# Kernel tuning notes

Measured on AMD Instinct MI355X. Metric: run time of the kernel, lower is better.

Reference implementation:

```python
import jax, jax.numpy as jnp
import numpy as np
from jax import lax


def conv2d(x, w, b, stride=1, pad=0):
    y = lax.conv_general_dilated(x, w, (stride, stride), [(pad, pad), (pad, pad)],
                                 dimension_numbers=('NCHW', 'OIHW', 'NCHW'))
    return y + b[None, :, None, None]


def squash(s, axis):
    # v = (|s|^2 / (1+|s|^2)) * s / |s|
    sq = jnp.sum(s * s, axis=axis, keepdims=True)
    return (sq / (1.0 + sq)) * s / jnp.sqrt(sq + 1e-9)


def conv_capsule(x, w, b_conv, caps_bias, out_dim, out_atoms, num_routing, stride, pad):
    # x: [B, in_dim, in_atoms, H, W]
    B, in_dim, in_atoms, H, W = x.shape
    xr = x.reshape(B * in_dim, in_atoms, H, W)
    conv = conv2d(xr, w, b_conv, stride, pad)              # [B*in_dim, out_dim*out_atoms, Ho, Wo]
    Ho, Wo = conv.shape[-2], conv.shape[-1]
    votes = conv.reshape(B, in_dim, out_dim, out_atoms, Ho, Wo)
    logits = jnp.zeros((B, in_dim, out_dim, Ho, Wo), dtype=x.dtype)
    act = None
    for i in range(num_routing):  # num_routing is a small static int (1 or 3)
        route = jax.nn.softmax(logits, axis=2)             # coupling over output capsules
        preact = jnp.einsum('bioHW,bioaHW->boaHW', route, votes) + caps_bias[None]
        act = squash(preact, axis=2)                        # [B, out_dim, out_atoms, Ho, Wo]
        if i < num_routing - 1:
            logits = logits + jnp.einsum('bioaHW,boaHW->bioHW', votes, act)
    return act


def forward(x, y, W1, b1, Wp, bp, cbp, Ws, bs, cbs, Wr1, br1, Wr2, br2, Wr3, br3):
    conv1 = jax.nn.relu(conv2d(x, W1, b1, 1, 2))                       # [B,256,H,W]
    primary = conv_capsule(conv1[:, None], Wp, bp, cbp, 32, 8, 1, 1, 2)  # [B,32,8,H,W]
    seg = conv_capsule(primary, Ws, bs, cbs, 1, 16, 3, 1, 0)             # [B,1,16,H,W]
    out_seg = jnp.sqrt(jnp.sum(seg * seg, axis=2) + 1e-9)                # Length: [B,1,H,W]
    masked = seg * y[:, :, None]                                         # Mask by label
    B, C, A, H, W = masked.shape
    r = masked.reshape(B * C, A, H, W)                                   # [B,16,H,W]
    r = jax.nn.relu(conv2d(r, Wr1, br1))
    r = jax.nn.relu(conv2d(r, Wr2, br2))
    out_recon = jax.nn.sigmoid(conv2d(r, Wr3, br3))                      # [B,1,H,W]
    return out_seg, out_recon


def setup_inputs():
    key = jax.random.key(0)
    ks = jax.random.split(key, 10)
    B, H, W = 2, 128, 128
    s = 0.05
    return {
        'x': jax.random.uniform(ks[0], (B, 1, H, W), jnp.float32),
        'y': (jax.random.uniform(ks[1], (B, 1, H, W)) > 0.5).astype(jnp.float32),
        'W1': jax.random.normal(ks[2], (256, 1, 5, 5), jnp.float32) * s,
        'b1': jnp.zeros((256,), jnp.float32),
        'Wp': jax.random.normal(ks[3], (256, 256, 5, 5), jnp.float32) * 0.01,
        'bp': jnp.zeros((256,), jnp.float32),
        'cbp': jnp.full((32, 8, 1, 1), 0.1, jnp.float32),
        'Ws': jax.random.normal(ks[4], (16, 8, 1, 1), jnp.float32) * s,
        'bs': jnp.zeros((16,), jnp.float32),
        'cbs': jnp.full((1, 16, 1, 1), 0.1, jnp.float32),
        'Wr1': jax.random.normal(ks[5], (64, 16, 1, 1), jnp.float32) * s,
        'br1': jnp.zeros((64,), jnp.float32),
        'Wr2': jax.random.normal(ks[6], (128, 64, 1, 1), jnp.float32) * s,
        'br2': jnp.zeros((128,), jnp.float32),
        'Wr3': jax.random.normal(ks[7], (1, 128, 1, 1), jnp.float32) * s,
        'br3': jnp.zeros((1,), jnp.float32),
    }


def reference(x, y, W1, b1, Wp, bp, cbp, Ws, bs, cbs, Wr1, br1, Wr2, br2, Wr3, br3):
    return forward(x, y, W1, b1, Wp, bp, cbp, Ws, bs, cbs, Wr1, br1, Wr2, br2, Wr3, br3)
```

## Files before the change

### kernel.cpp

```cpp
#include <hip/hip_runtime.h>
#include <hip/hip_bf16.h>

typedef __attribute__((ext_vector_type(8))) unsigned short us8;
typedef __attribute__((ext_vector_type(8))) __bf16 bf16x8;
typedef __attribute__((ext_vector_type(4))) float f32x4;

__device__ __forceinline__ unsigned short f2bf(float f) {
  unsigned int u = __float_as_uint(f);
  u += 0x7FFFu + ((u >> 16) & 1u);
  return (unsigned short)(u >> 16);
}
__device__ __forceinline__ float bf2f(unsigned short u) {
  return __uint_as_float(((unsigned int)u) << 16);
}

__device__ __forceinline__ void gld16(const unsigned short* g, unsigned short* l) {
  __builtin_amdgcn_global_load_lds(reinterpret_cast<const unsigned int*>(g),
                                   reinterpret_cast<unsigned int*>(l), 16, 0, 0);
}

#define APAD_BYTES 17842176
#define BT_OFF     17842176
#define PP_OFF     21118976

__global__ __launch_bounds__(256) void halo_zero(unsigned short* __restrict__ Apad) {
  int idx = blockIdx.x * 256 + threadIdx.x;
  int t8 = idx & 31;
  int pix = idx >> 5;
  int hw = pix % 17424;
  int h = hw / 132, w = hw - h * 132;
  if (h < 2 || h >= 130 || w < 2 || w >= 130) {
    us8 z = {0, 0, 0, 0, 0, 0, 0, 0};
    *(us8*)(Apad + (size_t)pix * 256 + t8 * 8) = z;
  }
}

__global__ __launch_bounds__(256) void prep_w(const float* __restrict__ Wp,
                                              unsigned short* __restrict__ BT) {
  __shared__ float w[6400];
  const int n = blockIdx.x;
  const float* src = Wp + n * 6400;
  for (int i = threadIdx.x; i < 6400; i += 256) w[i] = src[i];
  __syncthreads();
  for (int k = threadIdx.x; k < 6400; k += 256) {
    int dhw = k >> 8, c = k & 255;
    BT[n * 6400 + k] = f2bf(w[c * 25 + dhw]);
  }
}

__global__ __launch_bounds__(256) void conv1_k(const float* __restrict__ x,
                                               const float* __restrict__ W1,
                                               const float* __restrict__ b1,
                                               unsigned short* __restrict__ Apad) {
  int t = threadIdx.x;
  int pxt = blockIdx.x >> 3;
  int cq  = blockIdx.x & 7;
  int px  = (pxt << 6) + (t & 63);
  int cg  = __builtin_amdgcn_readfirstlane(t >> 6);
  int co0 = (cq << 5) + (cg << 3);
  int b = px >> 14, hw = px & 16383;
  int h = hw >> 7, w = hw & 127;

  float patch[25];
#pragma unroll
  for (int dh = 0; dh < 5; ++dh)
#pragma unroll
    for (int dw = 0; dw < 5; ++dw) {
      int hh = h + dh - 2, ww = w + dw - 2;
      bool ok = (hh >= 0) & (hh < 128) & (ww >= 0) & (ww < 128);
      patch[dh * 5 + dw] = ok ? x[(b << 14) + hh * 128 + ww] : 0.f;
    }
  us8 o;
#pragma unroll
  for (int c = 0; c < 8; ++c) {
    float acc = b1[co0 + c];
#pragma unroll
    for (int i = 0; i < 25; ++i) acc += patch[i] * W1[(co0 + c) * 25 + i];
    o[c] = f2bf(fmaxf(acc, 0.f));
  }
  *(us8*)(Apad + (size_t)((b * 132 + h + 2) * 132 + (w + 2)) * 256 + co0) = o;
}

#define STAGE_A(slot, ku) do { int dhw_=(ku)>>3, dh_=dhw_/5, dw_=dhw_-dh_*5;   \
    int ao_=((dh_*132+dw_)<<8)+(((ku)&7)<<5);                                  \
    gld16(Aap+abase0+ao_, &As[slot][sA]);                                      \
    gld16(Aap+abase1+ao_, &As[slot][sA+4096]); } while(0)
#define STAGE_B(slot, ku) do { int kp_=(ku)<<5;                                \
    gld16(BT+bbase0+kp_, &Bs[slot][sA]);                                       \
    gld16(BT+bbase1+kp_, &Bs[slot][sA+4096]); } while(0)
#define RDA(slot, s) (*(const bf16x8*)(&As[slot][areadbase + (s)*512]))
#define RDB(slot, j) (*(const bf16x8*)(&Bs[slot][breadbase + (j)*512]))
#define MFMA_Q(aset, bset, rb) do {                                            \
  _Pragma("unroll") for (int s_ = 0; s_ < 4; ++s_)                             \
  _Pragma("unroll") for (int j_ = 0; j_ < 4; ++j_)                             \
    acc[(rb)+s_][j_] = __builtin_amdgcn_mfma_f32_16x16x32_bf16(                \
        aset[s_], bset[j_], acc[(rb)+s_][j_], 0, 0, 0); } while(0)
#define BAR() __builtin_amdgcn_s_barrier()
#define VMC(n) asm volatile("s_waitcnt vmcnt(" #n ")" ::: "memory")

__global__ __launch_bounds__(512, 2) void caps_conv2(
    const unsigned short* __restrict__ Aap,
    const unsigned short* __restrict__ BT,
    unsigned short* __restrict__ Pp)
{
  __shared__ __attribute__((aligned(16))) unsigned short As[4][8192];
  __shared__ __attribute__((aligned(16))) unsigned short Bs[4][8192];

  const int tid = threadIdx.x;
  const int bid = blockIdx.x;
  const int lid = (bid & 7) * 32 + (bid >> 3);
  const int kid = lid & 1;
  const int m0 = (lid >> 1) << 8;
  const int t0 = kid * 100;
  const int wid = tid >> 6;
  const int l = tid & 63;

  const int swz = (l & 3) ^ ((l >> 3) & 3);
  int abase0, abase1, bbase0, bbase1;
  {
    int ra = wid * 16 + (l >> 2);
    int m = m0 + ra;
    int b = m >> 14, hw = m & 16383, h = hw >> 7, w = hw & 127;
    abase0 = ((b * 132 + h) * 132 + w) * 256 + swz * 8;
    m = m0 + ra + 128;
    b = m >> 14; hw = m & 16383; h = hw >> 7; w = hw & 127;
    abase1 = ((b * 132 + h) * 132 + w) * 256 + swz * 8;
    bbase0 = ra * 6400 + swz * 8;
    bbase1 = (ra + 128) * 6400 + swz * 8;
  }
  const int sA = wid * 512;

  const int rl = l & 15, q = l >> 4;
  const int wm = wid >> 2, wn = wid & 3;
  const int areadbase = (wm * 128 + rl) * 32 + ((q ^ ((rl >> 1) & 3)) << 3);
  const int breadbase = (wn * 64 + rl) * 32 + ((q ^ ((rl >> 1) & 3)) << 3);

  f32x4 acc[8][4] = {};
  bf16x8 aL[2][4], aH[4], bB[2][4];

  STAGE_A(0, t0 + 0); STAGE_B(0, t0 + 0);
  STAGE_A(1, t0 + 1); STAGE_B(1, t0 + 1);
  STAGE_A(2, t0 + 2); STAGE_B(2, t0 + 2);
  VMC(8); BAR();
#pragma unroll
  for (int s = 0; s < 4; ++s) aL[0][s] = RDA(0, s);
#pragma unroll
  for (int j = 0; j < 4; ++j) bB[0][j] = RDB(0, j);

  for (int it = 0; it < 24; ++it) {
    const int ub = t0 + it * 4;
#pragma unroll
    for (int sub = 0; sub < 4; ++sub) {
      const int par = sub & 1, nxt = par ^ 1;
      const int sU = sub, sU1 = (sub + 1) & 3, sS = (sub + 3) & 3;
#pragma unroll
      for (int s = 0; s < 4; ++s) aH[s] = RDA(sU, 4 + s);
      STAGE_A(sS, ub + sub + 3);
      VMC(6); BAR();
      __builtin_amdgcn_s_setprio(1);
      MFMA_Q(aL[par], bB[par], 0);
      __builtin_amdgcn_s_setprio(0);
      BAR();
#pragma unroll
      for (int s = 0; s < 4; ++s) aL[nxt][s] = RDA(sU1, s);
#pragma unroll
      for (int j = 0; j < 4; ++j) bB[nxt][j] = RDB(sU1, j);
      STAGE_B(sS, ub + sub + 3);
      BAR();
      __builtin_amdgcn_s_setprio(1);
      MFMA_Q(aH, bB[par], 4);
      __builtin_amdgcn_s_setprio(0);
      BAR();
    }
  }

#pragma unroll
  for (int s = 0; s < 4; ++s) aH[s] = RDA(0, 4 + s);
  STAGE_A(3, t0 + 99);
  VMC(6); BAR();
  __builtin_amdgcn_s_setprio(1); MFMA_Q(aL[0], bB[0], 0);
  __builtin_amdgcn_s_setprio(0); BAR();
#pragma unroll
  for (int s = 0; s < 4; ++s) aL[1][s] = RDA(1, s);
#pragma unroll
  for (int j = 0; j < 4; ++j) bB[1][j] = RDB(1, j);
  STAGE_B(3, t0 + 99);
  BAR();
  __builtin_amdgcn_s_setprio(1); MFMA_Q(aH, bB[0], 4);
  __builtin_amdgcn_s_setprio(0); BAR();
#pragma unroll
  for (int s = 0; s < 4; ++s) aH[s] = RDA(1, 4 + s);
  VMC(4); BAR();
  MFMA_Q(aL[1], bB[1], 0); BAR();
#pragma unroll
  for (int s = 0; s < 4; ++s) aL[0][s] = RDA(2, s);
#pragma unroll
  for (int j = 0; j < 4; ++j) bB[0][j] = RDB(2, j);
  BAR();
  MFMA_Q(aH, bB[1], 4); BAR();
#pragma unroll
  for (int s = 0; s < 4; ++s) aH[s] = RDA(2, 4 + s);
  VMC(0); BAR();
  MFMA_Q(aL[0], bB[0], 0); BAR();
#pragma unroll
  for (int s = 0; s < 4; ++s) aL[1][s] = RDA(3, s);
#pragma unroll
  for (int j = 0; j < 4; ++j) bB[1][j] = RDB(3, j);
  BAR();
  MFMA_Q(aH, bB[0], 4); BAR();
#pragma unroll
  for (int s = 0; s < 4; ++s) aH[s] = RDA(3, 4 + s);
  MFMA_Q(aL[1], bB[1], 0);
  MFMA_Q(aH, bB[1], 4);

  unsigned short* P = Pp + kid * 8388608;
#pragma unroll
  for (int s = 0; s < 8; ++s) {
#pragma unroll
    for (int j = 0; j < 4; ++j) {
      int col = wn * 64 + j * 16 + rl;
      int mrow = m0 + wm * 128 + s * 16 + (q << 2);
#pragma unroll
      for (int e = 0; e < 4; ++e)
        P[(size_t)(mrow + e) * 256 + col] = f2bf(acc[s][j][e]);
    }
  }
}

__global__ __launch_bounds__(128) void tail_k2(
    const unsigned short* __restrict__ Pp, const float* __restrict__ y,
    const float* __restrict__ bp, const float* __restrict__ cbp,
    const float* __restrict__ Ws, const float* __restrict__ bs,
    const float* __restrict__ cbs,
    const float* __restrict__ Wr1, const float* __restrict__ br1,
    const float* __restrict__ Wr2, const float* __restrict__ br2,
    const float* __restrict__ Wr3, const float* __restrict__ br3,
    float* __restrict__ out) {
  __shared__ float ccl[256];
  __shared__ float sbl[16];
  __shared__ float Wsl[128];
  __shared__ float W1l[1024];
  __shared__ float b1l[64];
  __shared__ float W2l[8192];
  __shared__ float b2l[128];
  __shared__ float W3l[128];

  const int tid = threadIdx.x;
  for (int i = tid; i < 256; i += 128) ccl[i] = bp[i] * (1.f / 32.f) + cbp[i];
  if (tid < 16) sbl[tid] = 32.f * bs[tid] + cbs[tid];
  if (tid < 128) { Wsl[tid] = Ws[tid]; b2l[tid] = br2[tid]; W3l[tid] = Wr3[tid]; }
  if (tid < 64) b1l[tid] = br1[tid];
  for (int i = tid; i < 1024; i += 128) W1l[i] = Wr1[i];
  for (int i = tid; i < 8192; i += 128) W2l[i] = Wr2[i];
  __syncthreads();

  const int m = blockIdx.x * 128 + tid;
  const us8* pr0 = (const us8*)(Pp + (size_t)m * 256);
  const us8* pr1 = (const us8*)(Pp + 8388608 + (size_t)m * 256);

  float P8[8] = {0.f, 0.f, 0.f, 0.f, 0.f, 0.f, 0.f, 0.f};
#pragma unroll 4
  for (int i = 0; i < 32; ++i) {
    us8 a = pr0[i], b = pr1[i];
    float v[8];
    float sq = 0.f;
#pragma unroll
    for (int c = 0; c < 8; ++c) {
      v[c] = (bf2f(a[c]) + bf2f(b[c])) * (1.f / 32.f) + ccl[i * 8 + c];
      sq += v[c] * v[c];
    }
    float scale = sq / ((1.f + sq) * sqrtf(sq + 1e-9f));
#pragma unroll
    for (int c = 0; c < 8; ++c) P8[c] += v[c] * scale;
  }

  float pre[16];
  float sq2 = 0.f;
#pragma unroll
  for (int a = 0; a < 16; ++a) {
    float s = sbl[a];
#pragma unroll
    for (int c = 0; c < 8; ++c) s += P8[c] * Wsl[a * 8 + c];
    pre[a] = s;
    sq2 += s * s;
  }
  float sc2 = sq2 / ((1.f + sq2) * sqrtf(sq2 + 1e-9f));
  out[m] = sqrtf(sq2 * sc2 * sc2 + 1e-9f);

  const float f = sc2 * y[m];
  float r1v[64];
#pragma unroll
  for (int j = 0; j < 64; ++j) {
    float s = b1l[j];
#pragma unroll
    for (int a = 0; a < 16; ++a) s += pre[a] * f * W1l[j * 16 + a];
    r1v[j] = fmaxf(s, 0.f);
  }
  float acc2 = br3[0];
  for (int k = 0; k < 128; ++k) {
    float s = b2l[k];
    const float4* wrow = (const float4*)(W2l + k * 64);
#pragma unroll
    for (int jj = 0; jj < 16; ++jj) {
      float4 wv = wrow[jj];
      s += r1v[jj * 4 + 0] * wv.x + r1v[jj * 4 + 1] * wv.y +
           r1v[jj * 4 + 2] * wv.z + r1v[jj * 4 + 3] * wv.w;
    }
    acc2 += fmaxf(s, 0.f) * W3l[k];
  }
  out[32768 + m] = 1.f / (1.f + expf(-acc2));
}

extern "C" void kernel_launch(void* const* d_in, const int* in_sizes, int n_in,
                              void* d_out, int out_size, void* d_ws, size_t ws_size,
                              hipStream_t stream) {
  const float* x   = (const float*)d_in[0];
  const float* y   = (const float*)d_in[1];
  const float* W1  = (const float*)d_in[2];
  const float* b1  = (const float*)d_in[3];
  const float* Wp  = (const float*)d_in[4];
  const float* bp  = (const float*)d_in[5];
  const float* cbp = (const float*)d_in[6];
  const float* Ws  = (const float*)d_in[7];
  const float* bs  = (const float*)d_in[8];
  const float* cbs = (const float*)d_in[9];
  const float* Wr1 = (const float*)d_in[10];
  const float* br1 = (const float*)d_in[11];
  const float* Wr2 = (const float*)d_in[12];
  const float* br2 = (const float*)d_in[13];
  const float* Wr3 = (const float*)d_in[14];
  const float* br3 = (const float*)d_in[15];
  float* out = (float*)d_out;

  char* ws = (char*)d_ws;
  unsigned short* Apad = (unsigned short*)ws;
  unsigned short* BT   = (unsigned short*)(ws + BT_OFF);
  unsigned short* Pp   = (unsigned short*)(ws + PP_OFF);

  hipLaunchKernelGGL(halo_zero, dim3(4356), dim3(256), 0, stream, Apad);
  hipLaunchKernelGGL(prep_w, dim3(256), dim3(256), 0, stream, Wp, BT);
  hipLaunchKernelGGL(conv1_k, dim3(4096), dim3(256), 0, stream, x, W1, b1, Apad);
  hipLaunchKernelGGL(caps_conv2, dim3(256), dim3(512), 0, stream, Apad, BT, Pp);
  hipLaunchKernelGGL(tail_k2, dim3(256), dim3(128), 0, stream,
                     Pp, y, bp, cbp, Ws, bs, cbs, Wr1, br1, Wr2, br2, Wr3, br3, out);
}
```

Before: 173.0 us.

## Merge prep kernels, hoist B-fragment LDS reads, split tail across thread pairs

Merges the halo-zeroing and weight-prep kernels into one launch, and the halo part now enumerates only border pixels instead of scanning every pixel. In the capsule conv GEMM main loop, the B-fragment LDS reads for the next step move ahead of the first MFMA barrier so they overlap with compute. The tail kernel uses two threads per output pixel, splitting the capsule reduction and the reconstruction MLP and exchanging partial results with shuffles, to raise parallelism and cut per-thread register use. In exchange it adds shuffle traffic and redundant per-thread work, and the reordered LDS reads may raise register pressure in the GEMM.

Result: faster. 162.7 us (-5.9%).

```diff
diff --git a/kernel.cpp b/kernel.cpp
--- a/kernel.cpp
+++ b/kernel.cpp
@@ -23,28 +23,38 @@
 #define BT_OFF     17842176
 #define PP_OFF     21118976
 
-__global__ __launch_bounds__(256) void halo_zero(unsigned short* __restrict__ Apad) {
-  int idx = blockIdx.x * 256 + threadIdx.x;
-  int t8 = idx & 31;
-  int pix = idx >> 5;
-  int hw = pix % 17424;
-  int h = hw / 132, w = hw - h * 132;
-  if (h < 2 || h >= 130 || w < 2 || w >= 130) {
+__global__ __launch_bounds__(256) void prep_halo(const float* __restrict__ Wp,
+                                                 unsigned short* __restrict__ BT,
+                                                 unsigned short* __restrict__ Apad) {
+  __shared__ float w[6400];
+  const int bid = blockIdx.x, tid = threadIdx.x;
+  if (bid < 256) {
+    const float* src = Wp + bid * 6400;
+    for (int i = tid; i < 6400; i += 256) w[i] = src[i];
+    __syncthreads();
+    for (int k = tid; k < 6400; k += 256) {
+      int dhw = k >> 8, c = k & 255;
+      BT[bid * 6400 + k] = f2bf(w[c * 25 + dhw]);
+    }
+  } else {
+    int idx = (bid - 256) * 256 + tid;
+    int chunk = idx & 31;
+    int pix = idx >> 5;
+    int img = pix >= 1040;
+    int p = pix - img * 1040;
+    int h, w2;
+    if (p < 528) {
+      int rs = p / 132;
+      h = (rs < 2) ? rs : rs + 128;
+      w2 = p - rs * 132;
+    } else {
+      int q = p - 528;
+      h = 2 + (q >> 2);
+      int cs = q & 3;
+      w2 = (cs < 2) ? cs : cs + 128;
+    }
     us8 z = {0, 0, 0, 0, 0, 0, 0, 0};
-    *(us8*)(Apad + (size_t)pix * 256 + t8 * 8) = z;
-  }
-}
-
-__global__ __launch_bounds__(256) void prep_w(const float* __restrict__ Wp,
-                                              unsigned short* __restrict__ BT) {
-  __shared__ float w[6400];
-  const int n = blockIdx.x;
-  const float* src = Wp + n * 6400;
-  for (int i = threadIdx.x; i < 6400; i += 256) w[i] = src[i];
-  __syncthreads();
-  for (int k = threadIdx.x; k < 6400; k += 256) {
-    int dhw = k >> 8, c = k & 255;
-    BT[n * 6400 + k] = f2bf(w[c * 25 + dhw]);
+    *(us8*)(Apad + (size_t)(img * 17424 + h * 132 + w2) * 256 + chunk * 8) = z;
   }
 }
 
@@ -156,15 +166,16 @@
 #pragma unroll
       for (int s = 0; s < 4; ++s) aH[s] = RDA(sU, 4 + s);
       STAGE_A(sS, ub + sub + 3);
-      VMC(6); BAR();
+      VMC(6);
+#pragma unroll
+      for (int j = 0; j < 4; ++j) bB[nxt][j] = RDB(sU1, j);
+      BAR();
       __builtin_amdgcn_s_setprio(1);
       MFMA_Q(aL[par], bB[par], 0);
       __builtin_amdgcn_s_setprio(0);
       BAR();
 #pragma unroll
       for (int s = 0; s < 4; ++s) aL[nxt][s] = RDA(sU1, s);
-#pragma unroll
-      for (int j = 0; j < 4; ++j) bB[nxt][j] = RDB(sU1, j);
       STAGE_B(sS, ub + sub + 3);
       BAR();
       __builtin_amdgcn_s_setprio(1);
@@ -177,35 +188,38 @@
 #pragma unroll
   for (int s = 0; s < 4; ++s) aH[s] = RDA(0, 4 + s);
   STAGE_A(3, t0 + 99);
-  VMC(6); BAR();
+  VMC(6);
+#pragma unroll
+  for (int j = 0; j < 4; ++j) bB[1][j] = RDB(1, j);
+  BAR();
   __builtin_amdgcn_s_setprio(1); MFMA_Q(aL[0], bB[0], 0);
   __builtin_amdgcn_s_setprio(0); BAR();
 #pragma unroll
   for (int s = 0; s < 4; ++s) aL[1][s] = RDA(1, s);
-#pragma unroll
-  for (int j = 0; j < 4; ++j) bB[1][j] = RDB(1, j);
   STAGE_B(3, t0 + 99);
   BAR();
   __builtin_amdgcn_s_setprio(1); MFMA_Q(aH, bB[0], 4);
   __builtin_amdgcn_s_setprio(0); BAR();
 #pragma unroll
   for (int s = 0; s < 4; ++s) aH[s] = RDA(1, 4 + s);
-  VMC(4); BAR();
+  VMC(4);
+#pragma unroll
+  for (int j = 0; j < 4; ++j) bB[0][j] = RDB(2, j);
+  BAR();
   MFMA_Q(aL[1], bB[1], 0); BAR();
 #pragma unroll
   for (int s = 0; s < 4; ++s) aL[0][s] = RDA(2, s);
-#pragma unroll
-  for (int j = 0; j < 4; ++j) bB[0][j] = RDB(2, j);
   BAR();
   MFMA_Q(aH, bB[1], 4); BAR();
 #pragma unroll
   for (int s = 0; s < 4; ++s) aH[s] = RDA(2, 4 + s);
-  VMC(0); BAR();
+  VMC(0);
+#pragma unroll
+  for (int j = 0; j < 4; ++j) bB[1][j] = RDB(3, j);
+  BAR();
   MFMA_Q(aL[0], bB[0], 0); BAR();
 #pragma unroll
   for (int s = 0; s < 4; ++s) aL[1][s] = RDA(3, s);
-#pragma unroll
-  for (int j = 0; j < 4; ++j) bB[1][j] = RDB(3, j);
   BAR();
   MFMA_Q(aH, bB[0], 4); BAR();
 #pragma unroll
@@ -227,7 +241,7 @@
   }
 }
 
-__global__ __launch_bounds__(128) void tail_k2(
+__global__ __launch_bounds__(256) void tail_k3(
     const unsigned short* __restrict__ Pp, const float* __restrict__ y,
     const float* __restrict__ bp, const float* __restrict__ cbp,
     const float* __restrict__ Ws, const float* __restrict__ bs,
@@ -246,69 +260,93 @@
   __shared__ float W3l[128];
 
   const int tid = threadIdx.x;
-  for (int i = tid; i < 256; i += 128) ccl[i] = bp[i] * (1.f / 32.f) + cbp[i];
+  ccl[tid] = bp[tid] * (1.f / 32.f) + cbp[tid];
   if (tid < 16) sbl[tid] = 32.f * bs[tid] + cbs[tid];
   if (tid < 128) { Wsl[tid] = Ws[tid]; b2l[tid] = br2[tid]; W3l[tid] = Wr3[tid]; }
   if (tid < 64) b1l[tid] = br1[tid];
-  for (int i = tid; i < 1024; i += 128) W1l[i] = Wr1[i];
-  for (int i = tid; i < 8192; i += 128) W2l[i] = Wr2[i];
+  for (int i = tid; i < 1024; i += 256) W1l[i] = Wr1[i];
+  for (int i = tid; i < 8192; i += 256) W2l[i] = Wr2[i];
   __syncthreads();
 
-  const int m = blockIdx.x * 128 + tid;
-  const us8* pr0 = (const us8*)(Pp + (size_t)m * 256);
-  const us8* pr1 = (const us8*)(Pp + 8388608 + (size_t)m * 256);
-
+  const int m = blockIdx.x * 128 + (tid >> 1);
+  const int hf = tid & 1;
+
+  const us8* pr0 = (const us8*)(Pp + (size_t)m * 256) + hf * 16;
+  const us8* pr1 = (const us8*)(Pp + 8388608 + (size_t)m * 256) + hf * 16;
   float P8[8] = {0.f, 0.f, 0.f, 0.f, 0.f, 0.f, 0.f, 0.f};
 #pragma unroll 4
-  for (int i = 0; i < 32; ++i) {
+  for (int i = 0; i < 16; ++i) {
     us8 a = pr0[i], b = pr1[i];
+    const int ci = (hf * 16 + i) * 8;
     float v[8];
-    float sq = 0.f;
-#pragma unroll
-    for (int c = 0; c < 8; ++c) {
-      v[c] = (bf2f(a[c]) + bf2f(b[c])) * (1.f / 32.f) + ccl[i * 8 + c];
-      sq += v[c] * v[c];
-    }
+#pragma unroll
+    for (int c = 0; c < 8; ++c)
+      v[c] = (bf2f(a[c]) + bf2f(b[c])) * (1.f / 32.f) + ccl[ci + c];
+    float sqa = v[0]*v[0] + v[1]*v[1] + v[2]*v[2] + v[3]*v[3];
+    float sqb = v[4]*v[4] + v[5]*v[5] + v[6]*v[6] + v[7]*v[7];
+    float sq = sqa + sqb;
     float scale = sq / ((1.f + sq) * sqrtf(sq + 1e-9f));
 #pragma unroll
     for (int c = 0; c < 8; ++c) P8[c] += v[c] * scale;
   }
+#pragma unroll
+  for (int c = 0; c < 8; ++c) P8[c] += __shfl_xor(P8[c], 1);
 
   float pre[16];
-  float sq2 = 0.f;
+  float sqx = 0.f, sqy = 0.f;
 #pragma unroll
   for (int a = 0; a < 16; ++a) {
-    float s = sbl[a];
-#pragma unroll
-    for (int c = 0; c < 8; ++c) s += P8[c] * Wsl[a * 8 + c];
+    float s0 = P8[0]*Wsl[a*8+0] + P8[1]*Wsl[a*8+1] + P8[2]*Wsl[a*8+2] + P8[3]*Wsl[a*8+3];
+    float s1 = P8[4]*Wsl[a*8+4] + P8[5]*Wsl[a*8+5] + P8[6]*Wsl[a*8+6] + P8[7]*Wsl[a*8+7];
+    float s = sbl[a] + s0 + s1;
     pre[a] = s;
-    sq2 += s * s;
-  }
+    if (a & 1) sqy += s * s; else sqx += s * s;
+  }
+  float sq2 = sqx + sqy;
   float sc2 = sq2 / ((1.f + sq2) * sqrtf(sq2 + 1e-9f));
-  out[m] = sqrtf(sq2 * sc2 * sc2 + 1e-9f);
+  if (hf == 0) out[m] = sqrtf(sq2 * sc2 * sc2 + 1e-9f);
 
   const float f = sc2 * y[m];
-  float r1v[64];
-#pragma unroll
-  for (int j = 0; j < 64; ++j) {
-    float s = b1l[j];
-#pragma unroll
-    for (int a = 0; a < 16; ++a) s += pre[a] * f * W1l[j * 16 + a];
-    r1v[j] = fmaxf(s, 0.f);
-  }
-  float acc2 = br3[0];
-  for (int k = 0; k < 128; ++k) {
-    float s = b2l[k];
-    const float4* wrow = (const float4*)(W2l + k * 64);
-#pragma unroll
-    for (int jj = 0; jj < 16; ++jj) {
-      float4 wv = wrow[jj];
-      s += r1v[jj * 4 + 0] * wv.x + r1v[jj * 4 + 1] * wv.y +
-           r1v[jj * 4 + 2] * wv.z + r1v[jj * 4 + 3] * wv.w;
-    }
-    acc2 += fmaxf(s, 0.f) * W3l[k];
-  }
-  out[32768 + m] = 1.f / (1.f + expf(-acc2));
+  float r1o[32];
+#pragma unroll
+  for (int jj = 0; jj < 32; ++jj) {
+    const float* wr = W1l + (hf * 32 + jj) * 16;
+    float s0 = 0.f, s1 = 0.f;
+#pragma unroll
+    for (int a = 0; a < 8; ++a) { s0 += pre[a] * f * wr[a]; s1 += pre[a+8] * f * wr[a+8]; }
+    r1o[jj] = fmaxf(b1l[hf * 32 + jj] + s0 + s1, 0.f);
+  }
+  float lo[32], hi[32];
+#pragma unroll
+  for (int jj = 0; jj < 32; ++jj) {
+    float tmp = __shfl_xor(r1o[jj], 1);
+    lo[jj] = hf ? tmp : r1o[jj];
+    hi[jj] = hf ? r1o[jj] : tmp;
+  }
+  float a0 = 0.f, a1 = 0.f, a2 = 0.f, a3 = 0.f;
+#pragma unroll 4
+  for (int kk = 0; kk < 64; ++kk) {
+    const int k = hf * 64 + kk;
+    const float* w = W2l + k * 64;
+    float s0 = 0.f, s1 = 0.f, s2 = 0.f, s3 = 0.f;
+#pragma unroll
+    for (int j = 0; j < 8; ++j) {
+      s0 += lo[j] * w[j];        s1 += lo[j + 8] * w[j + 8];
+      s2 += lo[j + 16] * w[j + 16]; s3 += lo[j + 24] * w[j + 24];
+    }
+#pragma unroll
+    for (int j = 0; j < 8; ++j) {
+      s0 += hi[j] * w[32 + j];        s1 += hi[j + 8] * w[40 + j];
+      s2 += hi[j + 16] * w[48 + j];   s3 += hi[j + 24] * w[56 + j];
+    }
+    float s = b2l[k] + (s0 + s1) + (s2 + s3);
+    float t = fmaxf(s, 0.f) * W3l[k];
+    switch (kk & 3) { case 0: a0 += t; break; case 1: a1 += t; break;
+                      case 2: a2 += t; break; default: a3 += t; }
+  }
+  float own = (a0 + a1) + (a2 + a3);
+  float acc2 = br3[0] + own + __shfl_xor(own, 1);
+  if (hf == 0) out[32768 + m] = 1.f / (1.f + expf(-acc2));
 }
 
 extern "C" void kernel_launch(void* const* d_in, const int* in_sizes, int n_in,
@@ -337,10 +375,9 @@
   unsigned short* BT   = (unsigned short*)(ws + BT_OFF);
   unsigned short* Pp   = (unsigned short*)(ws + PP_OFF);
 
-  hipLaunchKernelGGL(halo_zero, dim3(4356), dim3(256), 0, stream, Apad);
-  hipLaunchKernelGGL(prep_w, dim3(256), dim3(256), 0, stream, Wp, BT);
+  hipLaunchKernelGGL(prep_halo, dim3(516), dim3(256), 0, stream, Wp, BT, Apad);
   hipLaunchKernelGGL(conv1_k, dim3(4096), dim3(256), 0, stream, x, W1, b1, Apad);
   hipLaunchKernelGGL(caps_conv2, dim3(256), dim3(512), 0, stream, Apad, BT, Pp);
-  hipLaunchKernelGGL(tail_k2, dim3(256), dim3(128), 0, stream,
+  hipLaunchKernelGGL(tail_k3, dim3(256), dim3(256), 0, stream,
                      Pp, y, bp, cbp, Ws, bs, cbs, Wr1, br1, Wr2, br2, Wr3, br3, out);
 }
```
